# Kernel tuning notes

Measured on AMD Instinct MI355X. Metric: run time of the kernel, lower is better.

## Reference

```python
import jax, jax.numpy as jnp
import numpy as np

N, D, K = 20000, 64, 32
EPS = 1e-5


def _knn_numpy(coords, k):
    # exact KNN, chunked; self is nearest (distance 0) -> index 0 column
    n = coords.shape[0]
    sq = (coords ** 2).sum(1)
    out = np.empty((n, k), np.int64)
    for s in range(0, n, 2000):
        c = coords[s:s + 2000]
        d = sq[None, :] - 2.0 * c @ coords.T  # row-constant term dropped
        part = np.argpartition(d, k - 1, axis=1)[:, :k]
        dp = np.take_along_axis(d, part, 1)
        order = np.argsort(dp, axis=1)
        out[s:s + 2000] = np.take_along_axis(part, order, 1)
    return out


def setup_inputs() -> dict:
    key = jax.random.key(0)
    ks = jax.random.split(key, 24)
    coords = jax.random.uniform(ks[0], (N, 3), dtype=jnp.float32) * 100.0
    feats = jax.random.normal(ks[1], (N, D), dtype=jnp.float32)
    knn_idx = jnp.asarray(_knn_numpy(np.asarray(coords), K + 1))  # [N, 33], self first

    def lin(k, fi, fo):
        return jax.random.normal(k, (fi, fo), dtype=jnp.float32) / np.sqrt(fi).astype(np.float32)

    def vec(k, fo):
        return jax.random.normal(k, (fo,), dtype=jnp.float32) * 0.01

    return {
        'coords': coords, 'feats': feats,
        'Wq': lin(ks[2], D, D), 'bq': vec(ks[3], D),
        'Wk': lin(ks[4], D, D), 'bk': vec(ks[5], D),
        'Wv': lin(ks[6], D, D), 'bv': vec(ks[7], D),
        'Wl1': lin(ks[8], 3, D), 'bl1': vec(ks[9], D),
        'Wl2': lin(ks[10], D, D), 'bl2': vec(ks[11], D),
        'Ww1': lin(ks[12], D, D), 'bw1': vec(ks[13], D),
        'Ww2': lin(ks[14], D, D), 'bw2': vec(ks[15], D),
        'g_att': jnp.ones((D,), jnp.float32), 'b_att': jnp.zeros((D,), jnp.float32),
        'Wsg': lin(ks[16], D + 3, D), 'bsg': vec(ks[17], D),
        'Wf': lin(ks[18], D, D), 'bf': vec(ks[19], D),
        'g_ff': jnp.ones((D,), jnp.float32), 'b_ff': jnp.zeros((D,), jnp.float32),
        'knn_idx': knn_idx,
    }


def _sparsemax_axis1(z):
    # sparsemax over axis=1 of [n, k, d] (matches torch Sparsemax(dim=1))
    zt = jnp.moveaxis(z, 1, -1)  # [n, d, k]
    z_sorted = jnp.flip(jnp.sort(zt, axis=-1), axis=-1)
    csum = jnp.cumsum(z_sorted, axis=-1)
    r = jnp.arange(1, zt.shape[-1] + 1, dtype=zt.dtype)
    support = 1.0 + r * z_sorted > csum
    k_sup = jnp.sum(support, axis=-1, keepdims=True)  # int, >=1
    tau = (jnp.take_along_axis(csum, k_sup - 1, axis=-1) - 1.0) / k_sup.astype(zt.dtype)
    return jnp.moveaxis(jnp.maximum(zt - tau, 0.0), -1, 1)


def _layernorm(x, g, b):
    m = jnp.mean(x, -1, keepdims=True)
    v = jnp.mean((x - m) ** 2, -1, keepdims=True)
    return g * (x - m) * jax.lax.rsqrt(v + EPS) + b


def reference(coords, feats, Wq, bq, Wk, bk, Wv, bv, Wl1, bl1, Wl2, bl2,
              Ww1, bw1, Ww2, bw2, g_att, b_att, Wsg, bsg, Wf, bf, g_ff, b_ff,
              knn_idx):
    n = feats.shape[0]
    # ---- RNSA (knn_points includes self: first K columns) ----
    idx = knn_idx[:, :K]                                   # [N, K]
    diff = coords[idx] - coords[:, None, :]                # [N, K, 3]
    fc = jax.nn.relu(diff @ Wl1 + bl1) @ Wl2 + bl2         # positional MLP [N, K, D]
    pe = fc + feats[idx]                                   # positional embedding
    Q = jax.nn.relu(feats @ Wq + bq)                       # [N, D]
    Kf = jax.nn.relu(pe @ Wk + bk)                         # [N, K, D]
    V = pe @ Wv + bv                                       # [N, K, D]
    rel = (Kf - Q[:, None, :]) * fc
    w = jax.nn.relu(rel @ Ww1 + bw1) @ Ww2 + bw2
    w = _sparsemax_axis1(w)                                # dropout: eval mode -> identity
    attn = jnp.einsum('nkd,nkd->nd', V, w)
    x_att = feats + attn                                   # RNSA residual (x + attended)
    x_att = x_att + feats                                  # outer residual in GraphFormer

    # ---- feed-forward: LayerNorm + SGConv(K=1) + linear + residual + LayerNorm ----
    h = _layernorm(x_att, g_att, b_att)
    x_in = jnp.concatenate([h, coords], axis=-1)           # [N, D+3]
    # knn_graph(loop=False): 32 nearest excluding self -> columns 1..32
    src = knn_idx[:, 1:K + 1].reshape(-1)
    dst = jnp.repeat(jnp.arange(n), K)
    self_idx = jnp.arange(n)
    src_all = jnp.concatenate([src, self_idx])             # gcn_norm adds self loops
    dst_all = jnp.concatenate([dst, self_idx])
    deg = jax.ops.segment_sum(jnp.ones_like(src_all, dtype=x_in.dtype), dst_all, num_segments=n)
    norm = jax.lax.rsqrt(deg[src_all] * deg[dst_all])
    agg = jax.ops.segment_sum(x_in[src_all] * norm[:, None], dst_all, num_segments=n)
    x_ff = agg @ Wsg + bsg
    x_ff = jax.nn.relu(x_ff)
    x_ff = x_ff @ Wf + bf                                  # dropout: eval -> identity
    x_out = x_ff + h
    return _layernorm(x_out, g_ff, b_ff)
```

## Files before the change

kernel.cpp:

```cpp
#include <hip/hip_runtime.h>

#define NPTS 20000
#define EPSF 1e-5f

typedef _Float16 half8 __attribute__((ext_vector_type(8)));
typedef float floatx4 __attribute__((ext_vector_type(4)));

__global__ void prep_weights(const float* __restrict__ W0, const float* __restrict__ W1,
                             const float* __restrict__ W2, const float* __restrict__ W3,
                             const float* __restrict__ W4, const float* __restrict__ W5,
                             _Float16* __restrict__ wtg) {
  const float* srcs[6] = {W0, W1, W2, W3, W4, W5};
  const float* src = srcs[blockIdx.x];
  _Float16* dst = wtg + blockIdx.x * 4096;
  int t = threadIdx.x;
#pragma unroll
  for (int i = 0; i < 16; ++i) {
    int lin = i * 256 + t;
    int k = lin >> 6, d = lin & 63;
    dst[d * 64 + (((k >> 3) ^ (d & 7)) << 3) + (k & 7)] = (_Float16)src[lin];
  }
}

__device__ __forceinline__ half8 ldWt(const _Float16* __restrict__ w,
                                      int c15, int g, int nt, int ks) {
  int c = nt * 16 + c15;
  int kg = ks * 4 + g;
  return *(const half8*)(w + c * 64 + ((kg ^ (c & 7)) << 3));
}

__device__ __forceinline__ void stC(float* __restrict__ Tw, int c15, int g,
                                    int mt, int nt, floatx4 v) {
  int col = nt * 16 + c15;
  int chunk = mt * 4 + g;
  *(floatx4*)(Tw + col * 32 + ((chunk ^ (col & 7)) << 2)) = v;
}

__device__ __forceinline__ floatx4 ldCread(const float* __restrict__ Tw,
                                           int c15, int g, int mt, int nt) {
  int col = nt * 16 + c15;
  int chunk = mt * 4 + g;
  return *(const floatx4*)(Tw + col * 32 + ((chunk ^ (col & 7)) << 2));
}

__device__ __forceinline__ half8 ldA(const float* __restrict__ Tw,
                                     int c15, int g, int mt, int ks) {
  int m = mt * 16 + c15;
  half8 r;
#pragma unroll
  for (int j = 0; j < 8; ++j) {
    int c = ks * 32 + g * 8 + j;
    r[j] = (_Float16)Tw[c * 32 + (((m >> 2) ^ j) << 2) + (m & 3)];
  }
  return r;
}

__device__ __forceinline__ void ldAfrags(const float* __restrict__ Tw,
                                         int c15, int g, half8 a[2][2]) {
#pragma unroll
  for (int mt = 0; mt < 2; ++mt)
#pragma unroll
    for (int ks = 0; ks < 2; ++ks) a[mt][ks] = ldA(Tw, c15, g, mt, ks);
}

__device__ __forceinline__ void domm(const _Float16* __restrict__ w,
                                     const half8 a[2][2], int c15, int g,
                                     floatx4 acc[2][4]) {
#pragma unroll
  for (int ks = 0; ks < 2; ++ks)
#pragma unroll
    for (int nt = 0; nt < 4; ++nt) {
      half8 b = ldWt(w, c15, g, nt, ks);
#pragma unroll
      for (int mt = 0; mt < 2; ++mt)
        acc[mt][nt] = __builtin_amdgcn_mfma_f32_16x16x32_f16(a[mt][ks], b, acc[mt][nt], 0, 0, 0);
    }
}

__global__ __launch_bounds__(256) void q_kernel(const float* __restrict__ feats,
                                                const float* __restrict__ bq,
                                                const _Float16* __restrict__ wtg,
                                                _Float16* __restrict__ Qh) {
  const int wv = threadIdx.x >> 6, lane = threadIdx.x & 63;
  const int c15 = lane & 15, g = lane >> 4;
  const int n0 = (blockIdx.x * 4 + wv) * 32;
  const _Float16* wq = wtg + 5 * 4096;

  half8 a[2][2];
#pragma unroll
  for (int mt = 0; mt < 2; ++mt) {
    int r = n0 + mt * 16 + c15;
    if (r > NPTS - 1) r = NPTS - 1;
#pragma unroll
    for (int ks = 0; ks < 2; ++ks) {
      const float* p = feats + (size_t)r * 64 + ks * 32 + g * 8;
      float4 u0 = *(const float4*)p, u1 = *(const float4*)(p + 4);
      a[mt][ks][0] = (_Float16)u0.x; a[mt][ks][1] = (_Float16)u0.y;
      a[mt][ks][2] = (_Float16)u0.z; a[mt][ks][3] = (_Float16)u0.w;
      a[mt][ks][4] = (_Float16)u1.x; a[mt][ks][5] = (_Float16)u1.y;
      a[mt][ks][6] = (_Float16)u1.z; a[mt][ks][7] = (_Float16)u1.w;
    }
  }
  floatx4 acc[2][4] = {};
  domm(wq, a, c15, g, acc);
#pragma unroll
  for (int nt = 0; nt < 4; ++nt) {
    float bqv = bq[nt * 16 + c15];
#pragma unroll
    for (int mt = 0; mt < 2; ++mt)
#pragma unroll
      for (int r = 0; r < 4; ++r) {
        int n = n0 + mt * 16 + g * 4 + r;
        if (n < NPTS)
          Qh[(size_t)n * 64 + nt * 16 + c15] = (_Float16)fmaxf(acc[mt][nt][r] + bqv, 0.f);
      }
  }
}

__global__ __launch_bounds__(256, 4) void attn_kernel(
    const float* __restrict__ coords, const float* __restrict__ feats,
    const float* __restrict__ bk, const float* __restrict__ bv,
    const float* __restrict__ Wl1, const float* __restrict__ bl1,
    const float* __restrict__ bl2, const float* __restrict__ bw1,
    const float* __restrict__ bw2, const float* __restrict__ g_att,
    const float* __restrict__ b_att, const int* __restrict__ knn,
    const _Float16* __restrict__ wtg, const _Float16* __restrict__ Qh,
    _Float16* __restrict__ h_out)
{
  __shared__ float Tsh[4][2048];
  const int wv = threadIdx.x >> 6, lane = threadIdx.x & 63;
  const int c15 = lane & 15, g = lane >> 4;
  const int n = blockIdx.x * 4 + wv;
  float* Tw = Tsh[wv];
  const int* row = knn + (size_t)n * 33;

  const _Float16* wt_l2 = wtg;
  const _Float16* wt_v  = wtg + 4096;
  const _Float16* wt_k  = wtg + 8192;
  const _Float16* wt_w1 = wtg + 12288;
  const _Float16* wt_w2 = wtg + 16384;

  half8 aH[2][2];
  {
    float cnx = coords[(size_t)n * 3], cny = coords[(size_t)n * 3 + 1],
          cnz = coords[(size_t)n * 3 + 2];
#pragma unroll
    for (int ks = 0; ks < 2; ++ks) {
      int c0 = ks * 32 + g * 8;
      float4 wx0 = *(const float4*)(Wl1 + c0),       wx1 = *(const float4*)(Wl1 + c0 + 4);
      float4 wy0 = *(const float4*)(Wl1 + 64 + c0),  wy1 = *(const float4*)(Wl1 + 64 + c0 + 4);
      float4 wz0 = *(const float4*)(Wl1 + 128 + c0), wz1 = *(const float4*)(Wl1 + 128 + c0 + 4);
      float4 bb0 = *(const float4*)(bl1 + c0),       bb1 = *(const float4*)(bl1 + c0 + 4);
      float wx[8] = {wx0.x,wx0.y,wx0.z,wx0.w,wx1.x,wx1.y,wx1.z,wx1.w};
      float wy[8] = {wy0.x,wy0.y,wy0.z,wy0.w,wy1.x,wy1.y,wy1.z,wy1.w};
      float wz[8] = {wz0.x,wz0.y,wz0.z,wz0.w,wz1.x,wz1.y,wz1.z,wz1.w};
      float bb[8] = {bb0.x,bb0.y,bb0.z,bb0.w,bb1.x,bb1.y,bb1.z,bb1.w};
#pragma unroll
      for (int mt = 0; mt < 2; ++mt) {
        int id = row[mt * 16 + c15];
        float dx = coords[(size_t)id * 3] - cnx;
        float dy = coords[(size_t)id * 3 + 1] - cny;
        float dz = coords[(size_t)id * 3 + 2] - cnz;
#pragma unroll
        for (int j = 0; j < 8; ++j)
          aH[mt][ks][j] = (_Float16)fmaxf(dx * wx[j] + dy * wy[j] + dz * wz[j] + bb[j], 0.f);
      }
    }
  }

  floatx4 fc[2][4] = {};
  domm(wt_l2, aH, c15, g, fc);
#pragma unroll
  for (int nt = 0; nt < 4; ++nt) {
    float b = bl2[nt * 16 + c15];
#pragma unroll
    for (int mt = 0; mt < 2; ++mt) fc[mt][nt] += b;
  }

#pragma unroll
  for (int mt = 0; mt < 2; ++mt) {
    int idr[4];
#pragma unroll
    for (int r = 0; r < 4; ++r) idr[r] = row[mt * 16 + g * 4 + r];
#pragma unroll
    for (int nt = 0; nt < 4; ++nt) {
      floatx4 pe;
#pragma unroll
      for (int r = 0; r < 4; ++r)
        pe[r] = fc[mt][nt][r] + feats[(size_t)idr[r] * 64 + nt * 16 + c15];
      stC(Tw, c15, g, mt, nt, pe);
    }
  }
  __builtin_amdgcn_wave_barrier();
  half8 aP[2][2];
  ldAfrags(Tw, c15, g, aP);

  {
    floatx4 KR[2][4] = {};
    domm(wt_k, aP, c15, g, KR);
    __builtin_amdgcn_wave_barrier();
#pragma unroll
    for (int nt = 0; nt < 4; ++nt) {
      float bkv = bk[nt * 16 + c15];
      float q4 = (float)Qh[(size_t)n * 64 + nt * 16 + c15];
#pragma unroll
      for (int mt = 0; mt < 2; ++mt) {
        floatx4 v;
#pragma unroll
        for (int r = 0; r < 4; ++r)
          v[r] = (fmaxf(KR[mt][nt][r] + bkv, 0.f) - q4) * fc[mt][nt][r];
        stC(Tw, c15, g, mt, nt, v);
      }
    }
  }
  __builtin_amdgcn_wave_barrier();
  half8 aR[2][2];
  ldAfrags(Tw, c15, g, aR);

  {
    floatx4 W1[2][4] = {};
    domm(wt_w1, aR, c15, g, W1);
    __builtin_amdgcn_wave_barrier();
#pragma unroll
    for (int nt = 0; nt < 4; ++nt) {
      float b = bw1[nt * 16 + c15];
#pragma unroll
      for (int mt = 0; mt < 2; ++mt) {
        floatx4 v;
#pragma unroll
        for (int r = 0; r < 4; ++r) v[r] = fmaxf(W1[mt][nt][r] + b, 0.f);
        stC(Tw, c15, g, mt, nt, v);
      }
    }
  }
  __builtin_amdgcn_wave_barrier();
  half8 aW[2][2];
  ldAfrags(Tw, c15, g, aW);

  {
    floatx4 WW[2][4] = {};
    domm(wt_w2, aW, c15, g, WW);
    __builtin_amdgcn_wave_barrier();
#pragma unroll
    for (int nt = 0; nt < 4; ++nt) {
      float b = bw2[nt * 16 + c15];
#pragma unroll
      for (int mt = 0; mt < 2; ++mt) stC(Tw, c15, g, mt, nt, WW[mt][nt] + b);
    }
  }
  __builtin_amdgcn_wave_barrier();

  floatx4 V[2][4] = {};
  domm(wt_v, aP, c15, g, V);
#pragma unroll
  for (int nt = 0; nt < 4; ++nt) {
    float b = bv[nt * 16 + c15];
#pragma unroll
    for (int mt = 0; mt < 2; ++mt) V[mt][nt] += b;
  }

  float a[32];
#pragma unroll
  for (int i = 0; i < 8; ++i) {
    floatx4 ch = *(const floatx4*)(Tw + lane * 32 + ((i ^ (lane & 7)) << 2));
#pragma unroll
    for (int r = 0; r < 4; ++r) a[i * 4 + r] = ch[r];
  }
#pragma unroll
  for (int size = 2; size <= 32; size <<= 1) {
#pragma unroll
    for (int stride = size >> 1; stride > 0; stride >>= 1) {
#pragma unroll
      for (int i = 0; i < 32; ++i) {
        int j = i ^ stride;
        if (j > i) {
          float x = a[i], y = a[j];
          float lo = fminf(x, y), hi = fmaxf(x, y);
          bool up = ((i & size) == 0);
          a[i] = up ? hi : lo;
          a[j] = up ? lo : hi;
        }
      }
    }
  }
  float csum = 0.f, csel = 0.f;
  int ksup = 1;
#pragma unroll
  for (int i = 0; i < 32; ++i) {
    csum += a[i];
    if (1.0f + (float)(i + 1) * a[i] > csum) { ksup = i + 1; csel = csum; }
  }
  float tau = (csel - 1.0f) / (float)ksup;

  float x4[4];
#pragma unroll
  for (int nt = 0; nt < 4; ++nt) {
    float t4 = __shfl(tau, nt * 16 + c15, 64);
    float ssum = 0.f;
#pragma unroll
    for (int mt = 0; mt < 2; ++mt) {
      floatx4 w4 = ldCread(Tw, c15, g, mt, nt);
#pragma unroll
      for (int r = 0; r < 4; ++r)
        ssum += fmaxf(w4[r] - t4, 0.f) * V[mt][nt][r];
    }
    ssum += __shfl_xor(ssum, 16, 64);
    ssum += __shfl_xor(ssum, 32, 64);
    x4[nt] = 2.f * feats[(size_t)n * 64 + nt * 16 + c15] + ssum;
  }

  float sum = x4[0] + x4[1] + x4[2] + x4[3];
  float sum2 = x4[0] * x4[0] + x4[1] * x4[1] + x4[2] * x4[2] + x4[3] * x4[3];
#pragma unroll
  for (int m = 1; m < 16; m <<= 1) {
    sum += __shfl_xor(sum, m, 64);
    sum2 += __shfl_xor(sum2, m, 64);
  }
  float mean = sum * (1.f / 64.f);
  float var = sum2 * (1.f / 64.f) - mean * mean;
  float inv = rsqrtf(var + EPSF);
  h_out[(size_t)n * 64 + lane] =
      (_Float16)(g_att[lane] * (x4[g] - mean) * inv + b_att[lane]);
}

__global__ __launch_bounds__(256) void gconv_kernel(
    const float* __restrict__ coords, const _Float16* __restrict__ h,
    const float* __restrict__ Wsg, const float* __restrict__ bsg,
    const float* __restrict__ Wf, const float* __restrict__ bf,
    const float* __restrict__ g_ff, const float* __restrict__ b_ff,
    const int* __restrict__ knn, float* __restrict__ out)
{
  const int wave = threadIdx.x >> 6, lane = threadIdx.x & 63;
  const int p0 = (blockIdx.x * 4 + wave) * 2, p1 = p0 + 1;
  if (p0 >= NPTS) return;

  const int* rowA = knn + (size_t)p0 * 33;
  const int* rowB = knn + (size_t)p1 * 33;
  float hA = (float)h[(size_t)p0 * 64 + lane];
  float hB = (float)h[(size_t)p1 * 64 + lane];
  float aggA = hA, aggB = hB;
#pragma unroll 8
  for (int k = 1; k <= 32; ++k) {
    aggA += (float)h[(size_t)rowA[k] * 64 + lane];
    aggB += (float)h[(size_t)rowB[k] * 64 + lane];
  }

  float cxA = 0.f, cyA = 0.f, czA = 0.f, cxB = 0.f, cyB = 0.f, czB = 0.f;
  if (lane <= 32) {
    int sA = (lane == 0) ? p0 : rowA[lane];
    int sB = (lane == 0) ? p1 : rowB[lane];
    cxA = coords[(size_t)sA * 3];  cyA = coords[(size_t)sA * 3 + 1]; czA = coords[(size_t)sA * 3 + 2];
    cxB = coords[(size_t)sB * 3];  cyB = coords[(size_t)sB * 3 + 1]; czB = coords[(size_t)sB * 3 + 2];
  }
#pragma unroll
  for (int m = 1; m < 64; m <<= 1) {
    cxA += __shfl_xor(cxA, m, 64); cyA += __shfl_xor(cyA, m, 64); czA += __shfl_xor(czA, m, 64);
    cxB += __shfl_xor(cxB, m, 64); cyB += __shfl_xor(cyB, m, 64); czB += __shfl_xor(czB, m, 64);
  }
  const float inv33 = 1.0f / 33.0f;
  aggA *= inv33; aggB *= inv33;
  cxA *= inv33; cyA *= inv33; czA *= inv33;
  cxB *= inv33; cyB *= inv33; czB *= inv33;

  float t1a = bsg[lane], t1b = t1a;
#pragma unroll 8
  for (int c = 0; c < 64; ++c) {
    float w = Wsg[c * 64 + lane];
    t1a += __shfl(aggA, c, 64) * w;
    t1b += __shfl(aggB, c, 64) * w;
  }
  {
    float w64 = Wsg[64 * 64 + lane], w65 = Wsg[65 * 64 + lane], w66 = Wsg[66 * 64 + lane];
    t1a += cxA * w64 + cyA * w65 + czA * w66;
    t1b += cxB * w64 + cyB * w65 + czB * w66;
  }
  t1a = fmaxf(t1a, 0.f); t1b = fmaxf(t1b, 0.f);

  float t2a = bf[lane], t2b = t2a;
#pragma unroll 8
  for (int c = 0; c < 64; ++c) {
    float w = Wf[c * 64 + lane];
    t2a += __shfl(t1a, c, 64) * w;
    t2b += __shfl(t1b, c, 64) * w;
  }

  float xa = t2a + hA, xb = t2b + hB;
  float sa = xa, sa2 = xa * xa, sb = xb, sb2 = xb * xb;
#pragma unroll
  for (int m = 1; m < 64; m <<= 1) {
    sa += __shfl_xor(sa, m, 64);  sa2 += __shfl_xor(sa2, m, 64);
    sb += __shfl_xor(sb, m, 64);  sb2 += __shfl_xor(sb2, m, 64);
  }
  float ma = sa * (1.f / 64.f), va = sa2 * (1.f / 64.f) - ma * ma;
  float mb = sb * (1.f / 64.f), vb = sb2 * (1.f / 64.f) - mb * mb;
  float gl = g_ff[lane], bl = b_ff[lane];
  out[(size_t)p0 * 64 + lane] = gl * (xa - ma) * rsqrtf(va + EPSF) + bl;
  out[(size_t)p1 * 64 + lane] = gl * (xb - mb) * rsqrtf(vb + EPSF) + bl;
}

extern "C" void kernel_launch(void* const* d_in, const int* in_sizes, int n_in,
                              void* d_out, int out_size, void* d_ws, size_t ws_size,
                              hipStream_t stream) {
  (void)in_sizes; (void)n_in; (void)out_size; (void)ws_size;
  const float* coords = (const float*)d_in[0];
  const float* feats  = (const float*)d_in[1];
  const float* Wq  = (const float*)d_in[2];  const float* bq  = (const float*)d_in[3];
  const float* Wk  = (const float*)d_in[4];  const float* bk  = (const float*)d_in[5];
  const float* Wv  = (const float*)d_in[6];  const float* bv  = (const float*)d_in[7];
  const float* Wl1 = (const float*)d_in[8];  const float* bl1 = (const float*)d_in[9];
  const float* Wl2 = (const float*)d_in[10]; const float* bl2 = (const float*)d_in[11];
  const float* Ww1 = (const float*)d_in[12]; const float* bw1 = (const float*)d_in[13];
  const float* Ww2 = (const float*)d_in[14]; const float* bw2 = (const float*)d_in[15];
  const float* g_att = (const float*)d_in[16]; const float* b_att = (const float*)d_in[17];
  const float* Wsg = (const float*)d_in[18]; const float* bsg = (const float*)d_in[19];
  const float* Wf  = (const float*)d_in[20]; const float* bf  = (const float*)d_in[21];
  const float* g_ff = (const float*)d_in[22]; const float* b_ff = (const float*)d_in[23];
  const int* knn = (const int*)d_in[24];

  _Float16* h   = (_Float16*)d_ws;
  _Float16* wtg = (_Float16*)((char*)d_ws + 2621440);
  _Float16* Qh  = (_Float16*)((char*)d_ws + 2621440 + 49152);
  float* out = (float*)d_out;

  prep_weights<<<dim3(6), dim3(256), 0, stream>>>(Wl2, Wv, Wk, Ww1, Ww2, Wq, wtg);
  q_kernel<<<dim3(157), dim3(256), 0, stream>>>(feats, bq, wtg, Qh);
  attn_kernel<<<dim3(NPTS / 4), dim3(256), 0, stream>>>(
      coords, feats, bk, bv, Wl1, bl1, bl2, bw1, bw2,
      g_att, b_att, knn, wtg, Qh, h);
  gconv_kernel<<<dim3(2500), dim3(256), 0, stream>>>(
      coords, h, Wsg, bsg, Wf, bf, g_ff, b_ff, knn, out);
}
```

Baseline: 245.2 us.

## Rewrite graph conv with MFMA tiles, merge weight prep into Q kernel

The gconv kernel now handles 32 points per wave. It gathers neighbour features as half8 vectors and runs both dense layers (Wsg, Wf) as fp16 MFMA matmuls through a swizzled shared-memory staging buffer, replacing the per-lane shuffle-based scalar matvecs. Weight preparation and the Q projection are merged into one launch, with Q reading its fp32 weights directly, which removes one kernel launch and the dependency between the two. The sparsemax sort in the attention kernel is moved ahead of the V matmul so they can overlap. The cost is fewer, larger gconv blocks (157 vs 2500), which may hurt latency hiding for the gather, and fp16 rounding in the gconv matmuls.

```diff
diff --git a/kernel.cpp b/kernel.cpp
--- a/kernel.cpp
+++ b/kernel.cpp
@@ -5,22 +5,6 @@
 
 typedef _Float16 half8 __attribute__((ext_vector_type(8)));
 typedef float floatx4 __attribute__((ext_vector_type(4)));
-
-__global__ void prep_weights(const float* __restrict__ W0, const float* __restrict__ W1,
-                             const float* __restrict__ W2, const float* __restrict__ W3,
-                             const float* __restrict__ W4, const float* __restrict__ W5,
-                             _Float16* __restrict__ wtg) {
-  const float* srcs[6] = {W0, W1, W2, W3, W4, W5};
-  const float* src = srcs[blockIdx.x];
-  _Float16* dst = wtg + blockIdx.x * 4096;
-  int t = threadIdx.x;
-#pragma unroll
-  for (int i = 0; i < 16; ++i) {
-    int lin = i * 256 + t;
-    int k = lin >> 6, d = lin & 63;
-    dst[d * 64 + (((k >> 3) ^ (d & 7)) << 3) + (k & 7)] = (_Float16)src[lin];
-  }
-}
 
 __device__ __forceinline__ half8 ldWt(const _Float16* __restrict__ w,
                                       int c15, int g, int nt, int ks) {
@@ -29,6 +13,15 @@
   return *(const half8*)(w + c * 64 + ((kg ^ (c & 7)) << 3));
 }
 
+__device__ __forceinline__ half8 ldWtF32(const float* __restrict__ W,
+                                         int c15, int g, int nt, int ks) {
+  int c = nt * 16 + c15;
+  half8 r;
+#pragma unroll
+  for (int j = 0; j < 8; ++j) r[j] = (_Float16)W[(ks * 32 + g * 8 + j) * 64 + c];
+  return r;
+}
+
 __device__ __forceinline__ void stC(float* __restrict__ Tw, int c15, int g,
                                     int mt, int nt, floatx4 v) {
   int col = nt * 16 + c15;
@@ -77,14 +70,30 @@
     }
 }
 
-__global__ __launch_bounds__(256) void q_kernel(const float* __restrict__ feats,
-                                                const float* __restrict__ bq,
-                                                const _Float16* __restrict__ wtg,
-                                                _Float16* __restrict__ Qh) {
+__global__ __launch_bounds__(256) void prep_q_kernel(
+    const float* __restrict__ Wl2, const float* __restrict__ Wv,
+    const float* __restrict__ Wk, const float* __restrict__ Ww1,
+    const float* __restrict__ Ww2, const float* __restrict__ Wsg,
+    const float* __restrict__ Wf, const float* __restrict__ Wq,
+    const float* __restrict__ feats, const float* __restrict__ bq,
+    _Float16* __restrict__ wtg, _Float16* __restrict__ Qh)
+{
+  if (blockIdx.x < 7) {
+    const float* srcs[7] = {Wl2, Wv, Wk, Ww1, Ww2, Wsg, Wf};
+    const float* src = srcs[blockIdx.x];
+    _Float16* dst = wtg + blockIdx.x * 4096;
+    int t = threadIdx.x;
+#pragma unroll
+    for (int i = 0; i < 16; ++i) {
+      int lin = i * 256 + t;
+      int k = lin >> 6, d = lin & 63;
+      dst[d * 64 + (((k >> 3) ^ (d & 7)) << 3) + (k & 7)] = (_Float16)src[lin];
+    }
+    return;
+  }
   const int wv = threadIdx.x >> 6, lane = threadIdx.x & 63;
   const int c15 = lane & 15, g = lane >> 4;
-  const int n0 = (blockIdx.x * 4 + wv) * 32;
-  const _Float16* wq = wtg + 5 * 4096;
+  const int n0 = ((blockIdx.x - 7) * 4 + wv) * 32;
 
   half8 a[2][2];
 #pragma unroll
@@ -102,7 +111,15 @@
     }
   }
   floatx4 acc[2][4] = {};
-  domm(wq, a, c15, g, acc);
+#pragma unroll
+  for (int ks = 0; ks < 2; ++ks)
+#pragma unroll
+    for (int nt = 0; nt < 4; ++nt) {
+      half8 b = ldWtF32(Wq, c15, g, nt, ks);
+#pragma unroll
+      for (int mt = 0; mt < 2; ++mt)
+        acc[mt][nt] = __builtin_amdgcn_mfma_f32_16x16x32_f16(a[mt][ks], b, acc[mt][nt], 0, 0, 0);
+    }
 #pragma unroll
   for (int nt = 0; nt < 4; ++nt) {
     float bqv = bq[nt * 16 + c15];
@@ -250,6 +267,42 @@
   }
   __builtin_amdgcn_wave_barrier();
 
+  float tau;
+  {
+    float a[32];
+#pragma unroll
+    for (int i = 0; i < 8; ++i) {
+      floatx4 ch = *(const floatx4*)(Tw + lane * 32 + ((i ^ (lane & 7)) << 2));
+#pragma unroll
+      for (int r = 0; r < 4; ++r) a[i * 4 + r] = ch[r];
+    }
+#pragma unroll
+    for (int size = 2; size <= 32; size <<= 1) {
+#pragma unroll
+      for (int stride = size >> 1; stride > 0; stride >>= 1) {
+#pragma unroll
+        for (int i = 0; i < 32; ++i) {
+          int j = i ^ stride;
+          if (j > i) {
+            float x = a[i], y = a[j];
+            float lo = fminf(x, y), hi = fmaxf(x, y);
+            bool up = ((i & size) == 0);
+            a[i] = up ? hi : lo;
+            a[j] = up ? lo : hi;
+          }
+        }
+      }
+    }
+    float csum = 0.f, csel = 0.f;
+    int ksup = 1;
+#pragma unroll
+    for (int i = 0; i < 32; ++i) {
+      csum += a[i];
+      if (1.0f + (float)(i + 1) * a[i] > csum) { ksup = i + 1; csel = csum; }
+    }
+    tau = (csel - 1.0f) / (float)ksup;
+  }
+
   floatx4 V[2][4] = {};
   domm(wt_v, aP, c15, g, V);
 #pragma unroll
@@ -258,39 +311,6 @@
 #pragma unroll
     for (int mt = 0; mt < 2; ++mt) V[mt][nt] += b;
   }
-
-  float a[32];
-#pragma unroll
-  for (int i = 0; i < 8; ++i) {
-    floatx4 ch = *(const floatx4*)(Tw + lane * 32 + ((i ^ (lane & 7)) << 2));
-#pragma unroll
-    for (int r = 0; r < 4; ++r) a[i * 4 + r] = ch[r];
-  }
-#pragma unroll
-  for (int size = 2; size <= 32; size <<= 1) {
-#pragma unroll
-    for (int stride = size >> 1; stride > 0; stride >>= 1) {
-#pragma unroll
-      for (int i = 0; i < 32; ++i) {
-        int j = i ^ stride;
-        if (j > i) {
-          float x = a[i], y = a[j];
-          float lo = fminf(x, y), hi = fmaxf(x, y);
-          bool up = ((i & size) == 0);
-          a[i] = up ? hi : lo;
-          a[j] = up ? lo : hi;
-        }
-      }
-    }
-  }
-  float csum = 0.f, csel = 0.f;
-  int ksup = 1;
-#pragma unroll
-  for (int i = 0; i < 32; ++i) {
-    csum += a[i];
-    if (1.0f + (float)(i + 1) * a[i] > csum) { ksup = i + 1; csel = csum; }
-  }
-  float tau = (csel - 1.0f) / (float)ksup;
 
   float x4[4];
 #pragma unroll
@@ -325,77 +345,123 @@
 
 __global__ __launch_bounds__(256) void gconv_kernel(
     const float* __restrict__ coords, const _Float16* __restrict__ h,
-    const float* __restrict__ Wsg, const float* __restrict__ bsg,
-    const float* __restrict__ Wf, const float* __restrict__ bf,
+    const _Float16* __restrict__ wtg, const float* __restrict__ Wsg,
+    const float* __restrict__ bsg, const float* __restrict__ bf,
     const float* __restrict__ g_ff, const float* __restrict__ b_ff,
     const int* __restrict__ knn, float* __restrict__ out)
 {
-  const int wave = threadIdx.x >> 6, lane = threadIdx.x & 63;
-  const int p0 = (blockIdx.x * 4 + wave) * 2, p1 = p0 + 1;
-  if (p0 >= NPTS) return;
-
-  const int* rowA = knn + (size_t)p0 * 33;
-  const int* rowB = knn + (size_t)p1 * 33;
-  float hA = (float)h[(size_t)p0 * 64 + lane];
-  float hB = (float)h[(size_t)p1 * 64 + lane];
-  float aggA = hA, aggB = hB;
-#pragma unroll 8
-  for (int k = 1; k <= 32; ++k) {
-    aggA += (float)h[(size_t)rowA[k] * 64 + lane];
-    aggB += (float)h[(size_t)rowB[k] * 64 + lane];
-  }
-
-  float cxA = 0.f, cyA = 0.f, czA = 0.f, cxB = 0.f, cyB = 0.f, czB = 0.f;
-  if (lane <= 32) {
-    int sA = (lane == 0) ? p0 : rowA[lane];
-    int sB = (lane == 0) ? p1 : rowB[lane];
-    cxA = coords[(size_t)sA * 3];  cyA = coords[(size_t)sA * 3 + 1]; czA = coords[(size_t)sA * 3 + 2];
-    cxB = coords[(size_t)sB * 3];  cyB = coords[(size_t)sB * 3 + 1]; czB = coords[(size_t)sB * 3 + 2];
-  }
-#pragma unroll
-  for (int m = 1; m < 64; m <<= 1) {
-    cxA += __shfl_xor(cxA, m, 64); cyA += __shfl_xor(cyA, m, 64); czA += __shfl_xor(czA, m, 64);
-    cxB += __shfl_xor(cxB, m, 64); cyB += __shfl_xor(cyB, m, 64); czB += __shfl_xor(czB, m, 64);
-  }
+  __shared__ float Tsh[4][2048];
+  const int wv = threadIdx.x >> 6, lane = threadIdx.x & 63;
+  const int c15 = lane & 15, g = lane >> 4;
+  const int wid = blockIdx.x * 4 + wv;
+  if (wid >= (NPTS + 31) / 32) return;
+  const int n0 = wid * 32;
+  float* Tw = Tsh[wv];
+  const _Float16* wt_sg = wtg + 5 * 4096;
+  const _Float16* wt_f  = wtg + 6 * 4096;
   const float inv33 = 1.0f / 33.0f;
-  aggA *= inv33; aggB *= inv33;
-  cxA *= inv33; cyA *= inv33; czA *= inv33;
-  cxB *= inv33; cyB *= inv33; czB *= inv33;
-
-  float t1a = bsg[lane], t1b = t1a;
-#pragma unroll 8
-  for (int c = 0; c < 64; ++c) {
-    float w = Wsg[c * 64 + lane];
-    t1a += __shfl(aggA, c, 64) * w;
-    t1b += __shfl(aggB, c, 64) * w;
-  }
-  {
-    float w64 = Wsg[64 * 64 + lane], w65 = Wsg[65 * 64 + lane], w66 = Wsg[66 * 64 + lane];
-    t1a += cxA * w64 + cyA * w65 + czA * w66;
-    t1b += cxB * w64 + cyB * w65 + czB * w66;
-  }
-  t1a = fmaxf(t1a, 0.f); t1b = fmaxf(t1b, 0.f);
-
-  float t2a = bf[lane], t2b = t2a;
-#pragma unroll 8
-  for (int c = 0; c < 64; ++c) {
-    float w = Wf[c * 64 + lane];
-    t2a += __shfl(t1a, c, 64) * w;
-    t2b += __shfl(t1b, c, 64) * w;
-  }
-
-  float xa = t2a + hA, xb = t2b + hB;
-  float sa = xa, sa2 = xa * xa, sb = xb, sb2 = xb * xb;
-#pragma unroll
-  for (int m = 1; m < 64; m <<= 1) {
-    sa += __shfl_xor(sa, m, 64);  sa2 += __shfl_xor(sa2, m, 64);
-    sb += __shfl_xor(sb, m, 64);  sb2 += __shfl_xor(sb2, m, 64);
-  }
-  float ma = sa * (1.f / 64.f), va = sa2 * (1.f / 64.f) - ma * ma;
-  float mb = sb * (1.f / 64.f), vb = sb2 * (1.f / 64.f) - mb * mb;
-  float gl = g_ff[lane], bl = b_ff[lane];
-  out[(size_t)p0 * 64 + lane] = gl * (xa - ma) * rsqrtf(va + EPSF) + bl;
-  out[(size_t)p1 * 64 + lane] = gl * (xb - mb) * rsqrtf(vb + EPSF) + bl;
+
+  float acc[2][2][8] = {};
+  float cxa[2], cya[2], cza[2];
+#pragma unroll
+  for (int mt = 0; mt < 2; ++mt) {
+    int p = n0 + mt * 16 + c15;
+    const int* row = knn + (size_t)p * 33;
+#pragma unroll 11
+    for (int k = 0; k < 33; ++k) {
+      int idx = (k == 0) ? p : row[k];
+      const _Float16* hp = h + (size_t)idx * 64 + g * 8;
+      half8 v0 = *(const half8*)hp;
+      half8 v1 = *(const half8*)(hp + 32);
+#pragma unroll
+      for (int j = 0; j < 8; ++j) {
+        acc[mt][0][j] += (float)v0[j];
+        acc[mt][1][j] += (float)v1[j];
+      }
+    }
+    float sx = 0.f, sy = 0.f, sz = 0.f;
+    for (int k = g; k < 33; k += 4) {
+      int idx = (k == 0) ? p : row[k];
+      sx += coords[(size_t)idx * 3];
+      sy += coords[(size_t)idx * 3 + 1];
+      sz += coords[(size_t)idx * 3 + 2];
+    }
+    sx += __shfl_xor(sx, 16, 64); sx += __shfl_xor(sx, 32, 64);
+    sy += __shfl_xor(sy, 16, 64); sy += __shfl_xor(sy, 32, 64);
+    sz += __shfl_xor(sz, 16, 64); sz += __shfl_xor(sz, 32, 64);
+    cxa[mt] = sx * inv33; cya[mt] = sy * inv33; cza[mt] = sz * inv33;
+  }
+
+  half8 aA[2][2];
+#pragma unroll
+  for (int mt = 0; mt < 2; ++mt)
+#pragma unroll
+    for (int ks = 0; ks < 2; ++ks)
+#pragma unroll
+      for (int j = 0; j < 8; ++j)
+        aA[mt][ks][j] = (_Float16)(acc[mt][ks][j] * inv33);
+
+  {
+    floatx4 C1[2][4] = {};
+    domm(wt_sg, aA, c15, g, C1);
+#pragma unroll
+    for (int nt = 0; nt < 4; ++nt) {
+      int col = nt * 16 + c15;
+      float b = bsg[col];
+      float w64 = Wsg[4096 + col], w65 = Wsg[4160 + col], w66 = Wsg[4224 + col];
+#pragma unroll
+      for (int mt = 0; mt < 2; ++mt) {
+        floatx4 v;
+#pragma unroll
+        for (int r = 0; r < 4; ++r) {
+          int src = g * 4 + r;
+          float cx = __shfl(cxa[mt], src, 64);
+          float cy = __shfl(cya[mt], src, 64);
+          float cz = __shfl(cza[mt], src, 64);
+          v[r] = fmaxf(C1[mt][nt][r] + b + cx * w64 + cy * w65 + cz * w66, 0.f);
+        }
+        stC(Tw, c15, g, mt, nt, v);
+      }
+    }
+  }
+  __builtin_amdgcn_wave_barrier();
+  half8 aT[2][2];
+  ldAfrags(Tw, c15, g, aT);
+
+  floatx4 C2[2][4] = {};
+  domm(wt_f, aT, c15, g, C2);
+#pragma unroll
+  for (int nt = 0; nt < 4; ++nt) {
+    float b = bf[nt * 16 + c15];
+#pragma unroll
+    for (int mt = 0; mt < 2; ++mt)
+#pragma unroll
+      for (int r = 0; r < 4; ++r)
+        C2[mt][nt][r] += b + (float)h[(size_t)(n0 + mt * 16 + g * 4 + r) * 64 + nt * 16 + c15];
+  }
+#pragma unroll
+  for (int mt = 0; mt < 2; ++mt)
+#pragma unroll
+    for (int r = 0; r < 4; ++r) {
+      float s = C2[mt][0][r] + C2[mt][1][r] + C2[mt][2][r] + C2[mt][3][r];
+      float s2 = C2[mt][0][r] * C2[mt][0][r] + C2[mt][1][r] * C2[mt][1][r] +
+                 C2[mt][2][r] * C2[mt][2][r] + C2[mt][3][r] * C2[mt][3][r];
+#pragma unroll
+      for (int m = 1; m < 16; m <<= 1) {
+        s += __shfl_xor(s, m, 64);
+        s2 += __shfl_xor(s2, m, 64);
+      }
+      float mean = s * (1.f / 64.f);
+      float var = s2 * (1.f / 64.f) - mean * mean;
+      float inv = rsqrtf(var + EPSF);
+      int prow = n0 + mt * 16 + g * 4 + r;
+#pragma unroll
+      for (int nt = 0; nt < 4; ++nt) {
+        int col = nt * 16 + c15;
+        out[(size_t)prow * 64 + col] =
+            g_ff[col] * (C2[mt][nt][r] - mean) * inv + b_ff[col];
+      }
+    }
 }
 
 extern "C" void kernel_launch(void* const* d_in, const int* in_sizes, int n_in,
@@ -419,14 +485,14 @@
 
   _Float16* h   = (_Float16*)d_ws;
   _Float16* wtg = (_Float16*)((char*)d_ws + 2621440);
-  _Float16* Qh  = (_Float16*)((char*)d_ws + 2621440 + 49152);
+  _Float16* Qh  = (_Float16*)((char*)d_ws + 2621440 + 57344);
   float* out = (float*)d_out;
 
-  prep_weights<<<dim3(6), dim3(256), 0, stream>>>(Wl2, Wv, Wk, Ww1, Ww2, Wq, wtg);
-  q_kernel<<<dim3(157), dim3(256), 0, stream>>>(feats, bq, wtg, Qh);
+  prep_q_kernel<<<dim3(164), dim3(256), 0, stream>>>(
+      Wl2, Wv, Wk, Ww1, Ww2, Wsg, Wf, Wq, feats, bq, wtg, Qh);
   attn_kernel<<<dim3(NPTS / 4), dim3(256), 0, stream>>>(
       coords, feats, bk, bv, Wl1, bl1, bl2, bw1, bw2,
       g_att, b_att, knn, wtg, Qh, h);
-  gconv_kernel<<<dim3(2500), dim3(256), 0, stream>>>(
-      coords, h, Wsg, bsg, Wf, bf, g_ff, b_ff, knn, out);
-}
+  gconv_kernel<<<dim3(157), dim3(256), 0, stream>>>(
+      coords, h, wtg, Wsg, bsg, bf, g_ff, b_ff, knn, out);
+}
```

Measured after the change: 230.0 us. -6.2%, faster.
